# Kernel tuning notes

Hardware: AMD Instinct MI355X
Metric: run time of the kernel (lower is better)

The kernel has to match this reference:

```python
import jax, jax.numpy as jnp
import numpy as np

B, N, T, D, H, K = 8, 100, 16, 4, 64, 2
E = N * (N - 1)  # 9900 directed edges (fully connected, no self-loops)


def setup_inputs() -> dict:
    key = jax.random.key(0)
    ks = jax.random.split(key, 12)
    inputs = jax.random.normal(ks[0], (B, N, T, D), jnp.float32)
    # edge-type distribution per directed pair (softmax over K types)
    rel_type = jax.nn.softmax(jax.random.normal(ks[1], (B, E, K), jnp.float32), axis=-1)
    # one-hot receiver / sender incidence matrices for fully-connected graph
    off = ~np.eye(N, dtype=bool)
    send_idx, rec_idx = np.where(off)
    eye = np.eye(N, dtype=np.float32)
    rel_rec = jnp.asarray(eye[rec_idx])    # [E, N]
    rel_send = jnp.asarray(eye[send_idx])  # [E, N]
    s = 0.1
    msg_fc1_w = jax.random.normal(ks[2], (K, H, 2 * D), jnp.float32) * s
    msg_fc1_b = jax.random.normal(ks[3], (K, H), jnp.float32) * s
    msg_fc2_w = jax.random.normal(ks[4], (K, H, H), jnp.float32) * s
    msg_fc2_b = jax.random.normal(ks[5], (K, H), jnp.float32) * s
    out_fc1_w = jax.random.normal(ks[6], (H, D + H), jnp.float32) * s
    out_fc1_b = jax.random.normal(ks[7], (H,), jnp.float32) * s
    out_fc2_w = jax.random.normal(ks[8], (H, H), jnp.float32) * s
    out_fc2_b = jax.random.normal(ks[9], (H,), jnp.float32) * s
    out_fc3_w = jax.random.normal(ks[10], (D, H), jnp.float32) * s
    out_fc3_b = jax.random.normal(ks[11], (D,), jnp.float32) * s
    return {
        "inputs": inputs, "rel_type": rel_type,
        "rel_rec": rel_rec, "rel_send": rel_send,
        "msg_fc1_w": msg_fc1_w, "msg_fc1_b": msg_fc1_b,
        "msg_fc2_w": msg_fc2_w, "msg_fc2_b": msg_fc2_b,
        "out_fc1_w": out_fc1_w, "out_fc1_b": out_fc1_b,
        "out_fc2_w": out_fc2_w, "out_fc2_b": out_fc2_b,
        "out_fc3_w": out_fc3_w, "out_fc3_b": out_fc3_b,
        "pred_steps": 1,
    }


def reference(inputs, rel_type, rel_rec, rel_send,
              msg_fc1_w, msg_fc1_b, msg_fc2_w, msg_fc2_b,
              out_fc1_w, out_fc1_b, out_fc2_w, out_fc2_b,
              out_fc3_w, out_fc3_b, pred_steps):
    # inputs: [B, N, T, D] -> [B, T, N, D]
    x = jnp.transpose(inputs, (0, 2, 1, 3))
    b, t, n, d = x.shape
    # rel_type: [B, E, K] -> [B, T, E, K]
    rt = jnp.broadcast_to(rel_type[:, None], (b, t, rel_type.shape[1], rel_type.shape[2]))

    def single_step(xs, rts):
        # gather endpoint states: [B, T', E, D]
        recv = jnp.einsum('en,btnd->bted', rel_rec, xs)
        send = jnp.einsum('en,btnd->bted', rel_send, xs)
        pre_msg = jnp.concatenate([send, recv], axis=-1)  # [B, T', E, 2D]
        # per-edge-type MLP, skipping edge type 0 (skip_first_edge_type=True)
        h1 = jax.nn.relu(jnp.einsum('btef,khf->btekh', pre_msg, msg_fc1_w[1:]) + msg_fc1_b[1:])
        h2 = jax.nn.relu(jnp.einsum('btekh,kgh->btekg', h1, msg_fc2_w[1:]) + msg_fc2_b[1:])
        # mask by edge-type weight and sum over types -> [B, T', E, H]
        all_msgs = jnp.einsum('btekh,btek->bteh', h2, rts[..., 1:])
        # aggregate messages at receivers: [B, T', N, H]
        agg = jnp.einsum('bteh,en->btnh', all_msgs, rel_rec)
        aug = jnp.concatenate([xs, agg], axis=-1)  # [B, T', N, D+H]
        p = jax.nn.relu(aug @ out_fc1_w.T + out_fc1_b)
        p = jax.nn.relu(p @ out_fc2_w.T + out_fc2_b)
        p = p @ out_fc3_w.T + out_fc3_b
        return xs + p

    last_pred = x[:, 0::pred_steps]
    curr_rt = rt[:, 0::pred_steps]
    preds = []
    for _ in range(pred_steps):
        last_pred = single_step(last_pred, curr_rt)
        preds.append(last_pred)
    tp = preds[0].shape[1]
    # interleave: output[:, i::pred_steps] = preds[i]
    output = jnp.stack(preds, axis=2).reshape(b, tp * pred_steps, n, d)
    pred_all = output[:, : t - 1]  # [B, T-1, N, D]
    return jnp.transpose(pred_all, (0, 2, 1, 3))  # [B, N, T-1, D]
```

## Files before the change

kernel.cpp:

```cpp
#include <hip/hip_runtime.h>
#include <hip/hip_fp16.h>

#define B_  8
#define N_  100
#define T_  16
#define TP_ 15
#define D_  4
#define H_  64
#define E_  9900
#define NG  25
#define ROWS 12000

#define WS_AIN 0u
#define WS_V   2304000u
#define WS_RTT 3840000u
#define WS_UBF 4198400u
#define WS_W2F 5928960u
#define WS_W1F 5937152u
#define WS_W2B 5949440u
#define WS_W3F 5957632u

typedef __attribute__((ext_vector_type(8))) _Float16 f16x8;
typedef __attribute__((ext_vector_type(4))) float f32x4;

__device__ __forceinline__ void gload_lds16(const void* g, void* lds) {
    __builtin_amdgcn_global_load_lds(
        (const __attribute__((address_space(1))) void*)g,
        (__attribute__((address_space(3))) void*)lds, 16, 0, 0);
}

__device__ __forceinline__ f16x8 relu_add8(uint4 u, uint4 v) {
    const f16x8 a = __builtin_bit_cast(f16x8, u);
    const f16x8 b = __builtin_bit_cast(f16x8, v);
    const f16x8 s = a + b;
    const f16x8 z = (f16x8)(_Float16)0;
    return __builtin_elementwise_max(s, z);
}

__global__ __launch_bounds__(256)
void nri_prep(const float* __restrict__ x, const float* __restrict__ rel,
              const float* __restrict__ w1, const float* __restrict__ b1,
              const float* __restrict__ w2, const float* __restrict__ f1w,
              const float* __restrict__ f2w, const float* __restrict__ f3w,
              __half* __restrict__ ubf, __half* __restrict__ v_h,
              float* __restrict__ rtt, __half* __restrict__ ain,
              __half* __restrict__ w2f, __half* __restrict__ w1f,
              __half* __restrict__ w2b, __half* __restrict__ w3f)
{
    const int lane = threadIdx.x & 63;
    const int wid  = blockIdx.x * 4 + (threadIdx.x >> 6);

    if (wid < ROWS) {
        const int nn = wid % N_;
        const int bt = wid / N_;
        const int t  = bt % TP_;
        const int b  = bt / TP_;
        const float4 ws4 = *(const float4*)(w1 + lane * 8);
        const float4 wr4 = *(const float4*)(w1 + lane * 8 + 4);
        const float4 xv  = *(const float4*)(x + (((size_t)b * N_ + nn) * T_ + t) * D_);
        const float u = ws4.x * xv.x + ws4.y * xv.y + ws4.z * xv.z + ws4.w * xv.w;
        const float v = wr4.x * xv.x + wr4.y * xv.y + wr4.z * xv.z + wr4.w * xv.w
                        + b1[lane];
        ubf[(size_t)bt * 7200 + nn * 72 + lane] = __float2half(u);
        v_h[(size_t)wid * 64 + lane] = __float2half(v);
        if (lane == 32) {
            const unsigned short h0 = __half_as_ushort(__float2half(xv.x));
            const unsigned short h1 = __half_as_ushort(__float2half(xv.y));
            const unsigned short h2 = __half_as_ushort(__float2half(xv.z));
            const unsigned short h3 = __half_as_ushort(__float2half(xv.w));
            uint2 p; p.x = (unsigned)h0 | ((unsigned)h1 << 16);
                     p.y = (unsigned)h2 | ((unsigned)h3 << 16);
            *(uint2*)(ain + (size_t)wid * 96 + 64) = p;
        } else if (lane >= 33 && lane < 40) {
            uint2 zz; zz.x = 0u; zz.y = 0u;
            *(uint2*)(ain + (size_t)wid * 96 + 68 + (lane - 33) * 4) = zz;
        }
    } else if (wid < ROWS + B_ * N_) {
        const int idx = wid - ROWS;
        const int n = idx % N_;
        const int b = idx / N_;
        float* dst = rtt + (size_t)idx * 112;
        const int ia  = lane + (lane >= n ? 1 : 0);
        const int eda = ia * (N_ - 1) + (n < ia ? n : n - 1);
        dst[lane] = rel[((size_t)b * E_ + eda) * 2 + 1];
        if (lane < 48) {
            const int e2 = 64 + lane;
            float rv = 0.f;
            if (e2 < N_ - 1) {
                const int ib  = e2 + (e2 >= n ? 1 : 0);
                const int edb = ib * (N_ - 1) + (n < ib ? n : n - 1);
                rv = rel[((size_t)b * E_ + edb) * 2 + 1];
            }
            dst[64 + lane] = rv;
        }
    } else {
        const int fid = wid - (ROWS + B_ * N_);
        const int g16 = lane & 15, q = lane >> 4;
        unsigned short h[8];
        if (fid < 8) {
            const int s = fid >> 2, nt = fid & 3;
            const int g = nt * 16 + g16;
            #pragma unroll
            for (int j = 0; j < 8; ++j)
                h[j] = __half_as_ushort(__float2half(
                    w2[(size_t)g * 64 + s * 32 + q * 8 + j]));
            uint4 pv; pv.x = h[0] | ((unsigned)h[1] << 16); pv.y = h[2] | ((unsigned)h[3] << 16);
                      pv.z = h[4] | ((unsigned)h[5] << 16); pv.w = h[6] | ((unsigned)h[7] << 16);
            *(uint4*)(w2f + fid * 512 + lane * 8) = pv;
        } else if (fid < 20) {
            const int f = fid - 8;
            const int s = f >> 2, nt = f & 3;
            const int g = nt * 16 + g16;
            #pragma unroll
            for (int j = 0; j < 8; ++j) {
                const int k = s * 32 + q * 8 + j;
                float v = 0.f;
                if (k < 64)       v = f1w[(size_t)g * 68 + 4 + k];
                else if (k < 68)  v = f1w[(size_t)g * 68 + (k - 64)];
                h[j] = __half_as_ushort(__float2half(v));
            }
            uint4 pv; pv.x = h[0] | ((unsigned)h[1] << 16); pv.y = h[2] | ((unsigned)h[3] << 16);
                      pv.z = h[4] | ((unsigned)h[5] << 16); pv.w = h[6] | ((unsigned)h[7] << 16);
            *(uint4*)(w1f + f * 512 + lane * 8) = pv;
        } else if (fid < 28) {
            const int f = fid - 20;
            const int s = f >> 2, nt = f & 3;
            const int g = nt * 16 + g16;
            #pragma unroll
            for (int j = 0; j < 8; ++j)
                h[j] = __half_as_ushort(__float2half(
                    f2w[(size_t)g * 64 + s * 32 + q * 8 + j]));
            uint4 pv; pv.x = h[0] | ((unsigned)h[1] << 16); pv.y = h[2] | ((unsigned)h[3] << 16);
                      pv.z = h[4] | ((unsigned)h[5] << 16); pv.w = h[6] | ((unsigned)h[7] << 16);
            *(uint4*)(w2b + f * 512 + lane * 8) = pv;
        } else if (fid == 28) {
            unsigned short hh[16];
            #pragma unroll
            for (int nt = 0; nt < 4; ++nt)
                #pragma unroll
                for (int d = 0; d < 4; ++d)
                    hh[nt * 4 + d] = __half_as_ushort(__float2half(
                        f3w[d * 64 + nt * 16 + g16]));
            uint4 p0, p1;
            p0.x = hh[0] | ((unsigned)hh[1] << 16);  p0.y = hh[2] | ((unsigned)hh[3] << 16);
            p0.z = hh[4] | ((unsigned)hh[5] << 16);  p0.w = hh[6] | ((unsigned)hh[7] << 16);
            p1.x = hh[8] | ((unsigned)hh[9] << 16);  p1.y = hh[10] | ((unsigned)hh[11] << 16);
            p1.z = hh[12] | ((unsigned)hh[13] << 16); p1.w = hh[14] | ((unsigned)hh[15] << 16);
            *(uint4*)(w3f + lane * 16) = p0;
            *(uint4*)(w3f + lane * 16 + 8) = p1;
        }
    }
}

__global__ __launch_bounds__(256)
void nri_agg(const __half* __restrict__ ubf, const __half* __restrict__ v_h,
             const float* __restrict__ rtt, const __half* __restrict__ w2f,
             const float* __restrict__ b2, __half* __restrict__ ain)
{
    __shared__ __half u_lds[7680];

    const int tid  = threadIdx.x;
    const int lane = tid & 63;
    const int w    = tid >> 6;
    const int bid  = blockIdx.x;
    const int g  = bid % NG;
    const int t  = (bid / NG) % TP_;
    const int b  = bid / (NG * TP_);
    const int bt = b * TP_ + t;

    {
        const char* gsrc = (const char*)(ubf + (size_t)bt * 7200);
        char* ldst = (char*)u_lds;
        #pragma unroll
        for (int j = 0; j < 4; ++j) {
            const int c = w + 4 * j;
            if (c < 15)
                gload_lds16(gsrc + c * 1024 + lane * 16, ldst + c * 1024);
        }
    }

    const int col = lane & 15;
    const int q   = lane >> 4;
    const int kq  = q * 8;

    f16x8 bfr[8];
    #pragma unroll
    for (int f = 0; f < 8; ++f)
        bfr[f] = *(const f16x8*)((const char*)w2f + f * 1024 + lane * 16);

    const int n   = g * 4 + w;
    const int row = bt * N_ + n;
    const __half* vp = v_h + (size_t)row * 64;
    const uint4 vv0 = *(const uint4*)(vp + kq);
    const uint4 vv1 = *(const uint4*)(vp + 32 + kq);
    float bb[4];
    #pragma unroll
    for (int nt = 0; nt < 4; ++nt) bb[nt] = b2[nt * 16 + col];
    const float* rtp = rtt + ((size_t)b * N_ + n) * 112 + q * 4;

    __syncthreads();

    float aggl[4] = {0.f, 0.f, 0.f, 0.f};
    #pragma unroll
    for (int mf = 0; mf < 7; ++mf) {
        const int e = mf * 16 + col;
        int i = e + (e >= n ? 1 : 0);
        if (i > N_ - 1) i = N_ - 1;
        const float4 rt4 = *(const float4*)(rtp + mf * 16);
        f32x4 acc[4] = {};
        const uint4 ud0 = *(const uint4*)&u_lds[i * 72 + kq];
        const f16x8 af0 = relu_add8(ud0, vv0);
        #pragma unroll
        for (int nt = 0; nt < 4; ++nt)
            acc[nt] = __builtin_amdgcn_mfma_f32_16x16x32_f16(af0, bfr[nt], acc[nt], 0, 0, 0);
        const uint4 ud1 = *(const uint4*)&u_lds[i * 72 + 32 + kq];
        const f16x8 af1 = relu_add8(ud1, vv1);
        #pragma unroll
        for (int nt = 0; nt < 4; ++nt)
            acc[nt] = __builtin_amdgcn_mfma_f32_16x16x32_f16(af1, bfr[4 + nt], acc[nt], 0, 0, 0);
        #pragma unroll
        for (int nt = 0; nt < 4; ++nt) {
            aggl[nt] += fmaxf(acc[nt][0] + bb[nt], 0.f) * rt4.x
                      + fmaxf(acc[nt][1] + bb[nt], 0.f) * rt4.y
                      + fmaxf(acc[nt][2] + bb[nt], 0.f) * rt4.z
                      + fmaxf(acc[nt][3] + bb[nt], 0.f) * rt4.w;
        }
    }
    #pragma unroll
    for (int nt = 0; nt < 4; ++nt) {
        float p = aggl[nt];
        p += __shfl_xor(p, 16, 64);
        p += __shfl_xor(p, 32, 64);
        if (lane < 16)
            ain[(size_t)row * 96 + nt * 16 + col] = __float2half(p);
    }
}

__global__ __launch_bounds__(256)
void nri_out(const __half* __restrict__ ain, const __half* __restrict__ w1f,
             const __half* __restrict__ w2b, const __half* __restrict__ w3f,
             const float* __restrict__ f1b, const float* __restrict__ f2b,
             const float* __restrict__ f3b, const float* __restrict__ x,
             float* __restrict__ out)
{
    __shared__ __half p1buf[4][16 * 72];

    const int tid  = threadIdx.x;
    const int lane = tid & 63;
    const int w    = tid >> 6;
    const int row0 = (blockIdx.x * 4 + w) * 16;
    if (row0 >= ROWS) return;

    const int col = lane & 15;
    const int q   = lane >> 4;
    const int kq  = q * 8;

    f16x8 w1r[12];
    #pragma unroll
    for (int f = 0; f < 12; ++f)
        w1r[f] = *(const f16x8*)((const char*)w1f + f * 1024 + lane * 16);
    f16x8 w2r[8];
    #pragma unroll
    for (int f = 0; f < 8; ++f)
        w2r[f] = *(const f16x8*)((const char*)w2b + f * 1024 + lane * 16);
    float b1v[4], b2v[4];
    #pragma unroll
    for (int nt = 0; nt < 4; ++nt) { b1v[nt] = f1b[nt * 16 + col]; b2v[nt] = f2b[nt * 16 + col]; }
    const float4 b3v = *(const float4*)f3b;
    float w3v[16];
    {
        const uint4 p0 = *(const uint4*)(w3f + col * 16);
        const uint4 p1 = *(const uint4*)(w3f + col * 16 + 8);
        const unsigned* pp0 = (const unsigned*)&p0;
        const unsigned* pp1 = (const unsigned*)&p1;
        #pragma unroll
        for (int i = 0; i < 4; ++i) {
            w3v[2*i]     = __half2float(__ushort_as_half((unsigned short)(pp0[i] & 0xffff)));
            w3v[2*i + 1] = __half2float(__ushort_as_half((unsigned short)(pp0[i] >> 16)));
            w3v[8 + 2*i]     = __half2float(__ushort_as_half((unsigned short)(pp1[i] & 0xffff)));
            w3v[8 + 2*i + 1] = __half2float(__ushort_as_half((unsigned short)(pp1[i] >> 16)));
        }
    }

    f32x4 acc1[4] = {};
    #pragma unroll
    for (int s = 0; s < 3; ++s) {
        const uint4 ad = *(const uint4*)(ain + (size_t)(row0 + col) * 96 + s * 32 + kq);
        const f16x8 af = __builtin_bit_cast(f16x8, ad);
        #pragma unroll
        for (int nt = 0; nt < 4; ++nt)
            acc1[nt] = __builtin_amdgcn_mfma_f32_16x16x32_f16(af, w1r[s * 4 + nt], acc1[nt], 0, 0, 0);
    }
    #pragma unroll
    for (int nt = 0; nt < 4; ++nt)
        #pragma unroll
        for (int j = 0; j < 4; ++j)
            p1buf[w][(q * 4 + j) * 72 + nt * 16 + col] =
                __float2half(fmaxf(acc1[nt][j] + b1v[nt], 0.f));
    asm volatile("s_waitcnt lgkmcnt(0)" ::: "memory");
    __builtin_amdgcn_wave_barrier();

    f32x4 acc2[4] = {};
    #pragma unroll
    for (int s = 0; s < 2; ++s) {
        const uint4 pd = *(const uint4*)&p1buf[w][col * 72 + s * 32 + kq];
        const f16x8 af = __builtin_bit_cast(f16x8, pd);
        #pragma unroll
        for (int nt = 0; nt < 4; ++nt)
            acc2[nt] = __builtin_amdgcn_mfma_f32_16x16x32_f16(af, w2r[s * 4 + nt], acc2[nt], 0, 0, 0);
    }
    float p2v[4][4];
    #pragma unroll
    for (int nt = 0; nt < 4; ++nt)
        #pragma unroll
        for (int j = 0; j < 4; ++j)
            p2v[nt][j] = fmaxf(acc2[nt][j] + b2v[nt], 0.f);

    float pr[4][4];
    #pragma unroll
    for (int d = 0; d < 4; ++d)
        #pragma unroll
        for (int j = 0; j < 4; ++j) {
            float s = w3v[0 * 4 + d] * p2v[0][j] + w3v[1 * 4 + d] * p2v[1][j]
                    + w3v[2 * 4 + d] * p2v[2][j] + w3v[3 * 4 + d] * p2v[3][j];
            s += __shfl_xor(s, 1, 64);
            s += __shfl_xor(s, 2, 64);
            s += __shfl_xor(s, 4, 64);
            s += __shfl_xor(s, 8, 64);
            pr[d][j] = s;
        }

    if (col == 0) {
        #pragma unroll
        for (int j = 0; j < 4; ++j) {
            const int rg = row0 + q * 4 + j;
            const int n  = rg % N_;
            const int bt = rg / N_;
            const int t  = bt % TP_;
            const int b  = bt / TP_;
            const float4 xv = *(const float4*)(x + (((size_t)b * N_ + n) * T_ + t) * D_);
            float4 o;
            o.x = xv.x + b3v.x + pr[0][j];
            o.y = xv.y + b3v.y + pr[1][j];
            o.z = xv.z + b3v.z + pr[2][j];
            o.w = xv.w + b3v.w + pr[3][j];
            *(float4*)(out + (((size_t)b * N_ + n) * TP_ + t) * D_) = o;
        }
    }
}

extern "C" void kernel_launch(void* const* d_in, const int* in_sizes, int n_in,
                              void* d_out, int out_size, void* d_ws, size_t ws_size,
                              hipStream_t stream) {
    const float* x   = (const float*)d_in[0];
    const float* rel = (const float*)d_in[1];
    const float* w1  = (const float*)d_in[4] + 1 * H_ * 2 * D_;
    const float* b1  = (const float*)d_in[5] + 1 * H_;
    const float* w2  = (const float*)d_in[6] + 1 * H_ * H_;
    const float* b2  = (const float*)d_in[7] + 1 * H_;
    const float* f1w = (const float*)d_in[8];
    const float* f1b = (const float*)d_in[9];
    const float* f2w = (const float*)d_in[10];
    const float* f2b = (const float*)d_in[11];
    const float* f3w = (const float*)d_in[12];
    const float* f3b = (const float*)d_in[13];
    float* out = (float*)d_out;

    unsigned char* ws = (unsigned char*)d_ws;
    __half* ain = (__half*)(ws + WS_AIN);
    __half* v_h = (__half*)(ws + WS_V);
    float*  rtt = (float*)(ws + WS_RTT);
    __half* ubf = (__half*)(ws + WS_UBF);
    __half* w2f = (__half*)(ws + WS_W2F);
    __half* w1f = (__half*)(ws + WS_W1F);
    __half* w2b = (__half*)(ws + WS_W2B);
    __half* w3f = (__half*)(ws + WS_W3F);

    nri_prep<<<dim3(3208), 256, 0, stream>>>(x, rel, w1, b1, w2, f1w, f2w, f3w,
                                             ubf, v_h, rtt, ain,
                                             w2f, w1f, w2b, w3f);
    nri_agg<<<dim3(B_ * TP_ * NG), 256, 0, stream>>>(ubf, v_h, rtt, w2f, b2, ain);
    nri_out<<<dim3((ROWS / 16 + 3) / 4), 256, 0, stream>>>(ain, w1f, w2b, w3f,
                                                           f1b, f2b, f3b, x, out);
}
```

Measured before the change: 39.57 us.

## Process two receiver nodes per wave to reuse staged sender tiles

Each wave now handles two receiver nodes (n0 and n0+4), so every block covers 8 receivers and the grid shrinks from 25 to 13 node groups. The sender features loaded from LDS and the weight fragments are shared across both receivers, which halves the number of blocks that stage the same sender data. The rel_type table is now indexed by sender id with a zero at the self-edge, removing the per-lane skip-index arithmetic, and the bias is folded into the MFMA accumulator initialisation. MFMA sections are wrapped in s_setprio. The trade-off is higher register pressure and fewer blocks, which could lower occupancy.

```diff
diff --git a/kernel.cpp b/kernel.cpp
--- a/kernel.cpp
+++ b/kernel.cpp
@@ -8,7 +8,7 @@
 #define D_  4
 #define H_  64
 #define E_  9900
-#define NG  25
+#define NG  13
 #define ROWS 12000
 
 #define WS_AIN 0u
@@ -80,18 +80,23 @@
         const int n = idx % N_;
         const int b = idx / N_;
         float* dst = rtt + (size_t)idx * 112;
-        const int ia  = lane + (lane >= n ? 1 : 0);
-        const int eda = ia * (N_ - 1) + (n < ia ? n : n - 1);
-        dst[lane] = rel[((size_t)b * E_ + eda) * 2 + 1];
+        {
+            const int i = lane;
+            float rv = 0.f;
+            if (i != n) {
+                const int e = i * (N_ - 1) + (n < i ? n : n - 1);
+                rv = rel[((size_t)b * E_ + e) * 2 + 1];
+            }
+            dst[i] = rv;
+        }
         if (lane < 48) {
-            const int e2 = 64 + lane;
+            const int i2 = 64 + lane;
             float rv = 0.f;
-            if (e2 < N_ - 1) {
-                const int ib  = e2 + (e2 >= n ? 1 : 0);
-                const int edb = ib * (N_ - 1) + (n < ib ? n : n - 1);
-                rv = rel[((size_t)b * E_ + edb) * 2 + 1];
+            if (i2 < N_ && i2 != n) {
+                const int e2 = i2 * (N_ - 1) + (n < i2 ? n : n - 1);
+                rv = rel[((size_t)b * E_ + e2) * 2 + 1];
             }
-            dst[64 + lane] = rv;
+            dst[i2] = rv;
         }
     } else {
         const int fid = wid - (ROWS + B_ * N_);
@@ -188,51 +193,94 @@
     for (int f = 0; f < 8; ++f)
         bfr[f] = *(const f16x8*)((const char*)w2f + f * 1024 + lane * 16);
 
-    const int n   = g * 4 + w;
-    const int row = bt * N_ + n;
-    const __half* vp = v_h + (size_t)row * 64;
-    const uint4 vv0 = *(const uint4*)(vp + kq);
-    const uint4 vv1 = *(const uint4*)(vp + 32 + kq);
+    const int n0 = g * 8 + w;
+    const int n1 = n0 + 4;
+    const bool have1 = (n1 < N_);
+    const int n1c = have1 ? n1 : n0;
+    const int row0 = bt * N_ + n0;
+    const int row1 = bt * N_ + n1c;
+
+    const __half* vp0 = v_h + (size_t)row0 * 64;
+    const __half* vp1 = v_h + (size_t)row1 * 64;
+    const uint4 vv00 = *(const uint4*)(vp0 + kq);
+    const uint4 vv01 = *(const uint4*)(vp0 + 32 + kq);
+    const uint4 vv10 = *(const uint4*)(vp1 + kq);
+    const uint4 vv11 = *(const uint4*)(vp1 + 32 + kq);
     float bb[4];
     #pragma unroll
     for (int nt = 0; nt < 4; ++nt) bb[nt] = b2[nt * 16 + col];
-    const float* rtp = rtt + ((size_t)b * N_ + n) * 112 + q * 4;
+    const float* rtp0 = rtt + ((size_t)b * N_ + n0) * 112 + q * 4;
+    const float* rtp1 = rtt + ((size_t)b * N_ + n1c) * 112 + q * 4;
 
     __syncthreads();
 
-    float aggl[4] = {0.f, 0.f, 0.f, 0.f};
+    float agg0[4] = {0.f, 0.f, 0.f, 0.f};
+    float agg1[4] = {0.f, 0.f, 0.f, 0.f};
     #pragma unroll
     for (int mf = 0; mf < 7; ++mf) {
-        const int e = mf * 16 + col;
-        int i = e + (e >= n ? 1 : 0);
-        if (i > N_ - 1) i = N_ - 1;
-        const float4 rt4 = *(const float4*)(rtp + mf * 16);
-        f32x4 acc[4] = {};
+        const int i = min(mf * 16 + col, N_ - 1);
         const uint4 ud0 = *(const uint4*)&u_lds[i * 72 + kq];
-        const f16x8 af0 = relu_add8(ud0, vv0);
-        #pragma unroll
-        for (int nt = 0; nt < 4; ++nt)
-            acc[nt] = __builtin_amdgcn_mfma_f32_16x16x32_f16(af0, bfr[nt], acc[nt], 0, 0, 0);
         const uint4 ud1 = *(const uint4*)&u_lds[i * 72 + 32 + kq];
-        const f16x8 af1 = relu_add8(ud1, vv1);
-        #pragma unroll
-        for (int nt = 0; nt < 4; ++nt)
-            acc[nt] = __builtin_amdgcn_mfma_f32_16x16x32_f16(af1, bfr[4 + nt], acc[nt], 0, 0, 0);
+        const float4 rt40 = *(const float4*)(rtp0 + mf * 16);
+        const float4 rt41 = *(const float4*)(rtp1 + mf * 16);
+
+        f32x4 acc0[4], acc1[4];
         #pragma unroll
         for (int nt = 0; nt < 4; ++nt) {
-            aggl[nt] += fmaxf(acc[nt][0] + bb[nt], 0.f) * rt4.x
-                      + fmaxf(acc[nt][1] + bb[nt], 0.f) * rt4.y
-                      + fmaxf(acc[nt][2] + bb[nt], 0.f) * rt4.z
-                      + fmaxf(acc[nt][3] + bb[nt], 0.f) * rt4.w;
+            acc0[nt][0] = bb[nt]; acc0[nt][1] = bb[nt];
+            acc0[nt][2] = bb[nt]; acc0[nt][3] = bb[nt];
+            acc1[nt][0] = bb[nt]; acc1[nt][1] = bb[nt];
+            acc1[nt][2] = bb[nt]; acc1[nt][3] = bb[nt];
+        }
+        const f16x8 a00 = relu_add8(ud0, vv00);
+        const f16x8 a10 = relu_add8(ud0, vv10);
+        const f16x8 a01 = relu_add8(ud1, vv01);
+        const f16x8 a11 = relu_add8(ud1, vv11);
+
+        __builtin_amdgcn_s_setprio(1);
+        #pragma unroll
+        for (int nt = 0; nt < 4; ++nt)
+            acc0[nt] = __builtin_amdgcn_mfma_f32_16x16x32_f16(a00, bfr[nt], acc0[nt], 0, 0, 0);
+        #pragma unroll
+        for (int nt = 0; nt < 4; ++nt)
+            acc1[nt] = __builtin_amdgcn_mfma_f32_16x16x32_f16(a10, bfr[nt], acc1[nt], 0, 0, 0);
+        #pragma unroll
+        for (int nt = 0; nt < 4; ++nt)
+            acc0[nt] = __builtin_amdgcn_mfma_f32_16x16x32_f16(a01, bfr[4 + nt], acc0[nt], 0, 0, 0);
+        #pragma unroll
+        for (int nt = 0; nt < 4; ++nt)
+            acc1[nt] = __builtin_amdgcn_mfma_f32_16x16x32_f16(a11, bfr[4 + nt], acc1[nt], 0, 0, 0);
+        __builtin_amdgcn_s_setprio(0);
+
+        #pragma unroll
+        for (int nt = 0; nt < 4; ++nt) {
+            agg0[nt] = fmaf(fmaxf(acc0[nt][0], 0.f), rt40.x, agg0[nt]);
+            agg0[nt] = fmaf(fmaxf(acc0[nt][1], 0.f), rt40.y, agg0[nt]);
+            agg0[nt] = fmaf(fmaxf(acc0[nt][2], 0.f), rt40.z, agg0[nt]);
+            agg0[nt] = fmaf(fmaxf(acc0[nt][3], 0.f), rt40.w, agg0[nt]);
+            agg1[nt] = fmaf(fmaxf(acc1[nt][0], 0.f), rt41.x, agg1[nt]);
+            agg1[nt] = fmaf(fmaxf(acc1[nt][1], 0.f), rt41.y, agg1[nt]);
+            agg1[nt] = fmaf(fmaxf(acc1[nt][2], 0.f), rt41.z, agg1[nt]);
+            agg1[nt] = fmaf(fmaxf(acc1[nt][3], 0.f), rt41.w, agg1[nt]);
         }
     }
     #pragma unroll
     for (int nt = 0; nt < 4; ++nt) {
-        float p = aggl[nt];
+        float p = agg0[nt];
         p += __shfl_xor(p, 16, 64);
         p += __shfl_xor(p, 32, 64);
         if (lane < 16)
-            ain[(size_t)row * 96 + nt * 16 + col] = __float2half(p);
+            ain[(size_t)row0 * 96 + nt * 16 + col] = __float2half(p);
+    }
+    if (have1) {
+        #pragma unroll
+        for (int nt = 0; nt < 4; ++nt) {
+            float p = agg1[nt];
+            p += __shfl_xor(p, 16, 64);
+            p += __shfl_xor(p, 32, 64);
+            if (lane < 16)
+                ain[(size_t)row1 * 96 + nt * 16 + col] = __float2half(p);
+        }
     }
 }
 
```

Measured after the change: 48.24 us. +21.9%, slower.
